# Kernel optimization log

Hardware: AMD Instinct MI355X
Metric: run time of the kernel (lower is better)

## Reference

```python
import jax, jax.numpy as jnp
import numpy as np

BN_EPS = 1e-5

def _batchnorm(z, gamma, beta):
    # training-mode BN over node axis, biased variance (matches torch normalization)
    mean = jnp.mean(z, axis=0)
    var = jnp.mean((z - mean) ** 2, axis=0)
    return (z - mean) * jax.lax.rsqrt(var + BN_EPS) * gamma + beta

def setup_inputs() -> dict:
    key = jax.random.key(0)
    N, E, D, L = 100000, 1000000, 128, 2
    ks = jax.random.split(key, 8)
    x = jax.random.normal(ks[0], (N, D), dtype=jnp.float32)
    edge_index = jax.random.randint(ks[1], (2, E), 0, N, dtype=jnp.int64)
    s = 1.0 / np.sqrt(D)
    W1 = jax.random.uniform(ks[2], (L, D, D), jnp.float32, -s, s)
    b1 = jax.random.uniform(ks[3], (L, D), jnp.float32, -s, s)
    W2 = jax.random.uniform(ks[4], (L, D, D), jnp.float32, -s, s)
    b2 = jax.random.uniform(ks[5], (L, D), jnp.float32, -s, s)
    g1 = jnp.ones((L, D), jnp.float32); bt1 = jnp.zeros((L, D), jnp.float32)
    g_out = jnp.ones((L, D), jnp.float32); bt_out = jnp.zeros((L, D), jnp.float32)
    eps = jnp.zeros((L,), jnp.float32)  # GIN eps, init 0
    return {"x": x, "edge_index": edge_index, "W1": W1, "b1": b1, "g1": g1,
            "bt1": bt1, "W2": W2, "b2": b2, "eps": eps, "g_out": g_out, "bt_out": bt_out}

def reference(x, edge_index, W1, b1, g1, bt1, W2, b2, eps, g_out, bt_out):
    N = x.shape[0]
    L = W1.shape[0]
    src, dst = edge_index[0], edge_index[1]
    h = x
    for l in range(L):
        # message: relu(x_j) gathered along edges; aggregate: scatter-add to dst
        msg = jax.nn.relu(h[src])                                  # [E, D]
        aggr = jax.ops.segment_sum(msg, dst, num_segments=N)       # [N, D]
        z = (1.0 + eps[l]) * h + aggr
        # GINConv MLP: Linear -> BN -> ReLU -> Linear
        z = z @ W1[l].T + b1[l]
        z = jax.nn.relu(_batchnorm(z, g1[l], bt1[l]))
        z = z @ W2[l].T + b2[l]
        # outer per-layer BatchNorm
        z = _batchnorm(z, g_out[l], bt_out[l])
        if l < L - 1:
            z = jax.nn.relu(z)
        # dropout is identity in eval mode
        h = z
    return h
```

## Files before the change

kernel.cpp:

```cpp
#include <hip/hip_runtime.h>

typedef unsigned int u32;
typedef unsigned short u16;
typedef __attribute__((ext_vector_type(8))) short bf16x8;
typedef __attribute__((ext_vector_type(4))) float f32x4;

#define DF 128
#define NBUCK 256
#define BUCK_SHIFT 9
#define BUCK_SIZE 512
#define P2_CHUNK 4096
#define NCOPY 16
#define STATW (NCOPY * DF)

__device__ __forceinline__ float bf2f(u32 h) { return __uint_as_float(h << 16); }
__device__ __forceinline__ u16 f2bf(float f) {
  u32 u = __float_as_uint(f);
  u32 r = (u + 0x7fffu + ((u >> 16) & 1u)) >> 16;
  return (u16)r;
}
__device__ __forceinline__ u32 pack2(float a, float b) {
  return (u32)f2bf(a) | ((u32)f2bf(b) << 16);
}

__global__ void k_cvt3(const float* __restrict__ x, const float* __restrict__ w1,
                       const float* __restrict__ w2, u16* __restrict__ xb,
                       u16* __restrict__ w1b, u16* __restrict__ w2b,
                       int n4x, int n4w) {
  int i = blockIdx.x * blockDim.x + threadIdx.x;
  const float* in; u16* out; int idx;
  if (i < n4x) { in = x; out = xb; idx = i; }
  else if (i < n4x + n4w) { in = w1; out = w1b; idx = i - n4x; }
  else if (i < n4x + 2 * n4w) { in = w2; out = w2b; idx = i - n4x - n4w; }
  else return;
  float4 v = ((const float4*)in)[idx];
  ((uint2*)out)[idx] = make_uint2(pack2(v.x, v.y), pack2(v.z, v.w));
}

__global__ __launch_bounds__(256) void k_p1(const int* __restrict__ dst,
                                            int* __restrict__ bucketCount, int E) {
  __shared__ int h[NBUCK];
  int t = threadIdx.x;
  h[t] = 0;
  __syncthreads();
  for (int e = blockIdx.x * 256 + t; e < E; e += gridDim.x * 256)
    atomicAdd(&h[((u32)dst[e]) >> BUCK_SHIFT], 1);
  __syncthreads();
  if (h[t]) atomicAdd(&bucketCount[t], h[t]);
}

__global__ __launch_bounds__(256) void k_pscan(const int* __restrict__ bucketCount,
                                               int* __restrict__ bucketStart,
                                               int* __restrict__ bucketCursor,
                                               int* __restrict__ rowptr, int N, int E) {
  __shared__ int sh[NBUCK];
  int t = threadIdx.x;
  int c = bucketCount[t];
  sh[t] = c;
  __syncthreads();
  for (int o = 1; o < 256; o <<= 1) {
    int v = (t >= o) ? sh[t - o] : 0;
    __syncthreads();
    sh[t] += v;
    __syncthreads();
  }
  int excl = sh[t] - c;
  bucketStart[t] = excl;
  bucketCursor[t] = excl;
  if (t == 255) { bucketStart[256] = sh[255]; rowptr[N] = E; }
}

__global__ __launch_bounds__(256) void k_p2(const int* __restrict__ src,
                                            const int* __restrict__ dst,
                                            int* __restrict__ bucketCursor,
                                            uint2* __restrict__ part, int E) {
  __shared__ int h[NBUCK], hs[NBUCK], base[NBUCK];
  __shared__ int total;
  __shared__ uint2 buf[P2_CHUNK];
  int t = threadIdx.x;
  int e0 = blockIdx.x * P2_CHUNK;
  h[t] = 0;
  __syncthreads();
  int myb[16], myr[16];
  uint2 mye[16];
  #pragma unroll
  for (int k = 0; k < 16; k++) {
    int e = e0 + k * 256 + t;
    myb[k] = -1;
    if (e < E) {
      int s = src[e], d = dst[e];
      mye[k] = make_uint2((u32)s, (u32)d);
      myb[k] = ((u32)d) >> BUCK_SHIFT;
      myr[k] = atomicAdd(&h[myb[k]], 1);
    }
  }
  __syncthreads();
  int hc = h[t];
  hs[t] = hc;
  __syncthreads();
  for (int o = 1; o < 256; o <<= 1) {
    int v = (t >= o) ? hs[t - o] : 0;
    __syncthreads();
    hs[t] += v;
    __syncthreads();
  }
  if (t == 255) total = hs[255];
  int excl = hs[t] - hc;
  base[t] = hc ? atomicAdd(&bucketCursor[t], hc) : 0;
  __syncthreads();
  hs[t] = excl;
  __syncthreads();
  #pragma unroll
  for (int k = 0; k < 16; k++)
    if (myb[k] >= 0) buf[hs[myb[k]] + myr[k]] = mye[k];
  __syncthreads();
  int tot = total;
  for (int i = t; i < tot; i += 256) {
    uint2 ed = buf[i];
    int b = ed.y >> BUCK_SHIFT;
    part[base[b] + (i - hs[b])] = ed;
  }
}

__global__ __launch_bounds__(256) void k_p3(const uint2* __restrict__ part,
                                            const int* __restrict__ bucketStart,
                                            int* __restrict__ rowptr,
                                            int* __restrict__ adj, int N) {
  __shared__ int deg[BUCK_SIZE], cur[BUCK_SIZE], psum[256];
  int b = blockIdx.x, t = threadIdx.x;
  int nodeBase = b << BUCK_SHIFT;
  int eb = bucketStart[b], ee = bucketStart[b + 1];
  deg[t] = 0; deg[t + 256] = 0;
  __syncthreads();
  for (int e = eb + t; e < ee; e += 256)
    atomicAdd(&deg[(int)part[e].y - nodeBase], 1);
  __syncthreads();
  int a0 = deg[2 * t], a1 = deg[2 * t + 1];
  psum[t] = a0 + a1;
  __syncthreads();
  for (int o = 1; o < 256; o <<= 1) {
    int v = (t >= o) ? psum[t - o] : 0;
    __syncthreads();
    psum[t] += v;
    __syncthreads();
  }
  int basep = psum[t] - (a0 + a1);
  int p0 = eb + basep, p1 = eb + basep + a0;
  cur[2 * t] = p0; cur[2 * t + 1] = p1;
  int n0 = nodeBase + 2 * t, n1 = nodeBase + 2 * t + 1;
  if (n0 < N) rowptr[n0] = p0;
  if (n1 < N) rowptr[n1] = p1;
  __syncthreads();
  for (int e = eb + t; e < ee; e += 256) {
    uint2 ed = part[e];
    int pos = atomicAdd(&cur[(int)ed.y - nodeBase], 1);
    adj[pos] = (int)ed.x;
  }
}

__global__ void k_aggr(const u16* __restrict__ h, const int* __restrict__ rowptr,
                       const int* __restrict__ adj, const float* __restrict__ epsArr,
                       int layer, int doRelu, u16* __restrict__ z, int N) {
  int wid = (blockIdx.x * blockDim.x + threadIdx.x) >> 6;
  if (wid >= N) return;
  int lane = threadIdx.x & 63;
  int g = lane >> 4, f = lane & 15;
  const uint4* h4 = (const uint4*)h;
  float e1 = 1.0f + epsArr[layer];

  f32x4 accLo = {0.f, 0.f, 0.f, 0.f}, accHi = {0.f, 0.f, 0.f, 0.f};

  if (g == 0) {
    uint4 v = h4[(size_t)wid * 16 + f];
    f32x4 lo = {__uint_as_float(v.x << 16), __uint_as_float(v.y << 16),
                __uint_as_float(v.z << 16), __uint_as_float(v.w << 16)};
    f32x4 hi = {__uint_as_float(v.x & 0xffff0000u), __uint_as_float(v.y & 0xffff0000u),
                __uint_as_float(v.z & 0xffff0000u), __uint_as_float(v.w & 0xffff0000u)};
    accLo = e1 * lo;
    accHi = e1 * hi;
  }

  int b = rowptr[wid], e = rowptr[wid + 1];
  for (int p = b; p < e; p += 8) {
    int i0 = p + g, i1 = p + 4 + g;
    uint4 v0 = make_uint4(0, 0, 0, 0), v1 = make_uint4(0, 0, 0, 0);
    if (i0 < e) v0 = h4[(size_t)(u32)adj[i0] * 16 + f];
    if (i1 < e) v1 = h4[(size_t)(u32)adj[i1] * 16 + f];
    u32 w0[4] = {v0.x, v0.y, v0.z, v0.w};
    u32 w1[4] = {v1.x, v1.y, v1.z, v1.w};
    if (doRelu) {
      #pragma unroll
      for (int k = 0; k < 4; k++) {
        u32 a = w0[k];
        if (a & 0x8000u)     a &= 0xffff0000u;
        if (a & 0x80000000u) a &= 0x0000ffffu;
        w0[k] = a;
        u32 bq = w1[k];
        if (bq & 0x8000u)     bq &= 0xffff0000u;
        if (bq & 0x80000000u) bq &= 0x0000ffffu;
        w1[k] = bq;
      }
    }
    f32x4 lo0 = {__uint_as_float(w0[0] << 16), __uint_as_float(w0[1] << 16),
                 __uint_as_float(w0[2] << 16), __uint_as_float(w0[3] << 16)};
    f32x4 hi0 = {__uint_as_float(w0[0] & 0xffff0000u), __uint_as_float(w0[1] & 0xffff0000u),
                 __uint_as_float(w0[2] & 0xffff0000u), __uint_as_float(w0[3] & 0xffff0000u)};
    f32x4 lo1 = {__uint_as_float(w1[0] << 16), __uint_as_float(w1[1] << 16),
                 __uint_as_float(w1[2] << 16), __uint_as_float(w1[3] << 16)};
    f32x4 hi1 = {__uint_as_float(w1[0] & 0xffff0000u), __uint_as_float(w1[1] & 0xffff0000u),
                 __uint_as_float(w1[2] & 0xffff0000u), __uint_as_float(w1[3] & 0xffff0000u)};
    accLo += lo0; accHi += hi0;
    accLo += lo1; accHi += hi1;
  }

  #pragma unroll
  for (int k = 0; k < 4; k++) {
    accLo[k] += __shfl_xor(accLo[k], 16);
    accLo[k] += __shfl_xor(accLo[k], 32);
    accHi[k] += __shfl_xor(accHi[k], 16);
    accHi[k] += __shfl_xor(accHi[k], 32);
  }
  if (g == 0) {
    uint4 o = make_uint4(pack2(accLo[0], accHi[0]), pack2(accLo[1], accHi[1]),
                         pack2(accLo[2], accHi[2]), pack2(accLo[3], accHi[3]));
    ((uint4*)z)[(size_t)wid * 16 + f] = o;
  }
}

__global__ __launch_bounds__(256, 3) void k_gemm(
    const u16* __restrict__ A, const u16* __restrict__ W, const float* __restrict__ bias,
    const float* __restrict__ pS, const float* __restrict__ pQ,
    const float* __restrict__ gamma, const float* __restrict__ beta, int trans,
    float* __restrict__ statS, float* __restrict__ statQ,
    u16* __restrict__ out, int Nrows) {
  __shared__ float sA[DF], sC[DF];
  int tid = threadIdx.x;
  if (trans) {
    if (tid < DF) {
      float S = 0.f, Q = 0.f;
      #pragma unroll
      for (int i = 0; i < NCOPY; i++) { S += pS[i * DF + tid]; Q += pQ[i * DF + tid]; }
      float inv_n = 1.0f / (float)Nrows;
      float mean = S * inv_n;
      float var = fmaxf(Q * inv_n - mean * mean, 0.0f);
      float iv = rsqrtf(var + 1e-5f);
      float av = gamma[tid] * iv;
      sA[tid] = av;
      sC[tid] = beta[tid] - mean * av;
    }
    __syncthreads();
  }

  int lane = tid & 63, w = tid >> 6;
  int rq = w >> 1, cq = w & 1;
  int m = lane & 15, quad = lane >> 4;
  int rowBase = blockIdx.x * 128;
  int lastRow = Nrows - 1;

  f32x4 acc[4][4];
  #pragma unroll
  for (int i = 0; i < 4; i++)
    #pragma unroll
    for (int j = 0; j < 4; j++) acc[i][j] = (f32x4){0.f, 0.f, 0.f, 0.f};

  #pragma unroll
  for (int kt = 0; kt < 4; kt++) {
    int gk = kt * 32 + quad * 8;
    bf16x8 af[4], bfr[4];
    #pragma unroll
    for (int i = 0; i < 4; i++) {
      int row = rowBase + (rq * 4 + i) * 16 + m;
      row = row < Nrows ? row : lastRow;
      af[i] = *(const bf16x8*)(A + (size_t)row * DF + gk);
    }
    #pragma unroll
    for (int j = 0; j < 4; j++)
      bfr[j] = *(const bf16x8*)(W + (size_t)((cq * 4 + j) * 16 + m) * DF + gk);
    if (trans) {
      f32x4 a0 = *(const f32x4*)(sA + gk), a1 = *(const f32x4*)(sA + gk + 4);
      f32x4 c0 = *(const f32x4*)(sC + gk), c1 = *(const f32x4*)(sC + gk + 4);
      #pragma unroll
      for (int i = 0; i < 4; i++) {
        bf16x8 v = af[i];
        #pragma unroll
        for (int k = 0; k < 8; k++) {
          float xk = __uint_as_float(((u32)(u16)v[k]) << 16);
          float ak = (k < 4) ? a0[k] : a1[k - 4];
          float ck = (k < 4) ? c0[k] : c1[k - 4];
          float r = fmaxf(fmaf(ak, xk, ck), 0.0f);
          v[k] = (short)f2bf(r);
        }
        af[i] = v;
      }
    }
    #pragma unroll
    for (int i = 0; i < 4; i++)
      #pragma unroll
      for (int j = 0; j < 4; j++)
        acc[i][j] = __builtin_amdgcn_mfma_f32_16x16x32_bf16(af[i], bfr[j], acc[i][j], 0, 0, 0);
  }

  float colS[4] = {0, 0, 0, 0}, colQ[4] = {0, 0, 0, 0};
  #pragma unroll
  for (int j = 0; j < 4; j++) {
    int col = (cq * 4 + j) * 16 + m;
    float bv = bias[col];
    #pragma unroll
    for (int i = 0; i < 4; i++) {
      int row0 = rowBase + (rq * 4 + i) * 16 + quad * 4;
      #pragma unroll
      for (int r = 0; r < 4; r++) {
        int row = row0 + r;
        if (row < Nrows) {
          float v = acc[i][j][r] + bv;
          out[(size_t)row * DF + col] = f2bf(v);
          colS[j] += v;
          colQ[j] += v * v;
        }
      }
    }
  }
  int copyOff = (blockIdx.x & (NCOPY - 1)) * DF;
  #pragma unroll
  for (int j = 0; j < 4; j++) {
    float s = colS[j], q = colQ[j];
    s += __shfl_xor(s, 16); q += __shfl_xor(q, 16);
    s += __shfl_xor(s, 32); q += __shfl_xor(q, 32);
    if (quad == 0) {
      int col = (cq * 4 + j) * 16 + m;
      atomicAdd(&statS[copyOff + col], s);
      atomicAdd(&statQ[copyOff + col], q);
    }
  }
}

__global__ void k_bnapply_bf16(const u16* __restrict__ u, const float* __restrict__ pS,
                               const float* __restrict__ pQ, const float* __restrict__ gamma,
                               const float* __restrict__ beta, u16* __restrict__ h,
                               int n8, int Nrows) {
  __shared__ float sA[DF], sC[DF];
  int t = threadIdx.x;
  if (t < DF) {
    float S = 0.f, Q = 0.f;
    #pragma unroll
    for (int i = 0; i < NCOPY; i++) { S += pS[i * DF + t]; Q += pQ[i * DF + t]; }
    float inv_n = 1.0f / (float)Nrows;
    float mean = S * inv_n;
    float var = fmaxf(Q * inv_n - mean * mean, 0.0f);
    float iv = rsqrtf(var + 1e-5f);
    float av = gamma[t] * iv;
    sA[t] = av;
    sC[t] = beta[t] - mean * av;
  }
  __syncthreads();
  int i = blockIdx.x * blockDim.x + t;
  if (i >= n8) return;
  int col = (i * 8) & 127;
  f32x4 a0 = *(const f32x4*)(sA + col), a1v = *(const f32x4*)(sA + col + 4);
  f32x4 c0 = *(const f32x4*)(sC + col), c1v = *(const f32x4*)(sC + col + 4);
  uint4 v = ((const uint4*)u)[i];
  float f0 = fmaxf(fmaf(a0[0], bf2f(v.x & 0xffffu), c0[0]), 0.f);
  float f1 = fmaxf(fmaf(a0[1], bf2f(v.x >> 16),     c0[1]), 0.f);
  float f2 = fmaxf(fmaf(a0[2], bf2f(v.y & 0xffffu), c0[2]), 0.f);
  float f3 = fmaxf(fmaf(a0[3], bf2f(v.y >> 16),     c0[3]), 0.f);
  float f4 = fmaxf(fmaf(a1v[0], bf2f(v.z & 0xffffu), c1v[0]), 0.f);
  float f5 = fmaxf(fmaf(a1v[1], bf2f(v.z >> 16),     c1v[1]), 0.f);
  float f6 = fmaxf(fmaf(a1v[2], bf2f(v.w & 0xffffu), c1v[2]), 0.f);
  float f7 = fmaxf(fmaf(a1v[3], bf2f(v.w >> 16),     c1v[3]), 0.f);
  ((uint4*)h)[i] = make_uint4(pack2(f0, f1), pack2(f2, f3), pack2(f4, f5), pack2(f6, f7));
}

__global__ void k_bnapply_f32(const u16* __restrict__ u, const float* __restrict__ pS,
                              const float* __restrict__ pQ, const float* __restrict__ gamma,
                              const float* __restrict__ beta, float* __restrict__ out,
                              int n8, int Nrows) {
  __shared__ float sA[DF], sC[DF];
  int t = threadIdx.x;
  if (t < DF) {
    float S = 0.f, Q = 0.f;
    #pragma unroll
    for (int i = 0; i < NCOPY; i++) { S += pS[i * DF + t]; Q += pQ[i * DF + t]; }
    float inv_n = 1.0f / (float)Nrows;
    float mean = S * inv_n;
    float var = fmaxf(Q * inv_n - mean * mean, 0.0f);
    float iv = rsqrtf(var + 1e-5f);
    float av = gamma[t] * iv;
    sA[t] = av;
    sC[t] = beta[t] - mean * av;
  }
  __syncthreads();
  int i = blockIdx.x * blockDim.x + t;
  if (i >= n8) return;
  int col = (i * 8) & 127;
  f32x4 a0 = *(const f32x4*)(sA + col), a1v = *(const f32x4*)(sA + col + 4);
  f32x4 c0 = *(const f32x4*)(sC + col), c1v = *(const f32x4*)(sC + col + 4);
  uint4 v = ((const uint4*)u)[i];
  float4 o0, o1;
  o0.x = fmaf(a0[0], bf2f(v.x & 0xffffu), c0[0]);
  o0.y = fmaf(a0[1], bf2f(v.x >> 16),     c0[1]);
  o0.z = fmaf(a0[2], bf2f(v.y & 0xffffu), c0[2]);
  o0.w = fmaf(a0[3], bf2f(v.y >> 16),     c0[3]);
  o1.x = fmaf(a1v[0], bf2f(v.z & 0xffffu), c1v[0]);
  o1.y = fmaf(a1v[1], bf2f(v.z >> 16),     c1v[1]);
  o1.z = fmaf(a1v[2], bf2f(v.w & 0xffffu), c1v[2]);
  o1.w = fmaf(a1v[3], bf2f(v.w >> 16),     c1v[3]);
  ((float4*)out)[i * 2] = o0;
  ((float4*)out)[i * 2 + 1] = o1;
}

extern "C" void kernel_launch(void* const* d_in, const int* in_sizes, int n_in,
                              void* d_out, int out_size, void* d_ws, size_t ws_size,
                              hipStream_t stream) {
  const float* x    = (const float*)d_in[0];
  const int*   ei   = (const int*)d_in[1];
  const float* W1   = (const float*)d_in[2];
  const float* b1   = (const float*)d_in[3];
  const float* g1   = (const float*)d_in[4];
  const float* bt1  = (const float*)d_in[5];
  const float* W2   = (const float*)d_in[6];
  const float* b2   = (const float*)d_in[7];
  const float* eps  = (const float*)d_in[8];
  const float* gout = (const float*)d_in[9];
  const float* btout= (const float*)d_in[10];

  int N = in_sizes[0] / DF;
  int E = in_sizes[1] / 2;
  int L = in_sizes[8];

  char* ws = (char*)d_ws;
  size_t off = 0;
  auto alloc = [&](size_t bytes) -> void* {
    void* p = ws + off;
    off += (bytes + 255) & ~(size_t)255;
    return p;
  };
  u16* Xb     = (u16*)alloc((size_t)N * DF * 2);
  u16* bufA   = (u16*)alloc((size_t)N * DF * 2);
  u16* bufB   = (u16*)alloc((size_t)N * DF * 2);
  int* rowptr = (int*)alloc((size_t)(N + 1) * 4);
  int* adj    = (int*)alloc((size_t)E * 4);
  uint2* part = (uint2*)alloc((size_t)E * 8);
  int* bCount = (int*)alloc(NBUCK * 4);
  int* bStart = (int*)alloc((NBUCK + 1) * 4);
  int* bCur   = (int*)alloc(NBUCK * 4);
  u16* W1b    = (u16*)alloc((size_t)L * DF * DF * 2);
  u16* W2b    = (u16*)alloc((size_t)L * DF * DF * 2);
  float* stats= (float*)alloc((size_t)L * 4 * STATW * 4);

  hipMemsetAsync(bCount, 0, NBUCK * 4, stream);
  hipMemsetAsync(stats, 0, (size_t)L * 4 * STATW * 4, stream);

  int n4x = N * DF / 4;
  int n4w = L * DF * DF / 4;
  int n4tot = n4x + 2 * n4w;
  k_cvt3<<<(n4tot + 255) / 256, 256, 0, stream>>>(x, W1, W2, Xb, W1b, W2b, n4x, n4w);

  const int* srcI = ei;
  const int* dstI = ei + E;
  int nbuckets = (N + BUCK_SIZE - 1) >> BUCK_SHIFT;
  k_p1<<<512, 256, 0, stream>>>(dstI, bCount, E);
  k_pscan<<<1, 256, 0, stream>>>(bCount, bStart, bCur, rowptr, N, E);
  k_p2<<<(E + P2_CHUNK - 1) / P2_CHUNK, 256, 0, stream>>>(srcI, dstI, bCur, part, E);
  k_p3<<<nbuckets, 256, 0, stream>>>(part, bStart, rowptr, adj, N);

  int gblocks = (N + 127) / 128;
  int n8 = N * DF / 8;
  for (int l = 0; l < L; l++) {
    float* S1 = stats + (size_t)(l * 4 + 0) * STATW;
    float* Q1 = stats + (size_t)(l * 4 + 1) * STATW;
    float* S2 = stats + (size_t)(l * 4 + 2) * STATW;
    float* Q2 = stats + (size_t)(l * 4 + 3) * STATW;
    const u16* H = (l == 0) ? Xb : bufB;
    k_aggr<<<(N + 3) / 4, 256, 0, stream>>>(H, rowptr, adj, eps, l,
                                            (l == 0) ? 1 : 0, bufA, N);
    k_gemm<<<gblocks, 256, 0, stream>>>(bufA, W1b + l * DF * DF, b1 + l * DF,
                                        nullptr, nullptr, nullptr, nullptr, 0,
                                        S1, Q1, bufB, N);
    k_gemm<<<gblocks, 256, 0, stream>>>(bufB, W2b + l * DF * DF, b2 + l * DF,
                                        S1, Q1, g1 + l * DF, bt1 + l * DF, 1,
                                        S2, Q2, bufA, N);
    if (l < L - 1) {
      k_bnapply_bf16<<<(n8 + 255) / 256, 256, 0, stream>>>(
          bufA, S2, Q2, gout + l * DF, btout + l * DF, bufB, n8, N);
    } else {
      k_bnapply_f32<<<(n8 + 255) / 256, 256, 0, stream>>>(
          bufA, S2, Q2, gout + l * DF, btout + l * DF, (float*)d_out, n8, N);
    }
  }
}
```

Baseline: 449.6 us.

## Fuse neighbor aggregation with first GEMM via shared-memory tile

Result: slower. 563.1 us (+25.2%).

```diff
diff --git a/kernel.cpp b/kernel.cpp
--- a/kernel.cpp
+++ b/kernel.cpp
@@ -6,6 +6,7 @@
 typedef __attribute__((ext_vector_type(4))) float f32x4;
 
 #define DF 128
+#define LDA 136
 #define NBUCK 256
 #define BUCK_SHIFT 9
 #define BUCK_SIZE 512
@@ -158,98 +159,171 @@
   }
 }
 
-__global__ void k_aggr(const u16* __restrict__ h, const int* __restrict__ rowptr,
-                       const int* __restrict__ adj, const float* __restrict__ epsArr,
-                       int layer, int doRelu, u16* __restrict__ z, int N) {
-  int wid = (blockIdx.x * blockDim.x + threadIdx.x) >> 6;
-  if (wid >= N) return;
-  int lane = threadIdx.x & 63;
-  int g = lane >> 4, f = lane & 15;
+__global__ __launch_bounds__(256, 3) void k_aggemm(
+    const u16* __restrict__ h, const int* __restrict__ rowptr,
+    const int* __restrict__ adj, const float* __restrict__ epsArr,
+    int layer, int doRelu,
+    const u16* __restrict__ W, const float* __restrict__ bias,
+    float* __restrict__ statS, float* __restrict__ statQ,
+    u16* __restrict__ out, int N) {
+  __shared__ u16 zt[128 * LDA];
+  int tid = threadIdx.x;
+  int lane = tid & 63, w = tid >> 6;
+  int rowBase = blockIdx.x * 128;
   const uint4* h4 = (const uint4*)h;
   float e1 = 1.0f + epsArr[layer];
 
-  f32x4 accLo = {0.f, 0.f, 0.f, 0.f}, accHi = {0.f, 0.f, 0.f, 0.f};
-
-  if (g == 0) {
-    uint4 v = h4[(size_t)wid * 16 + f];
-    f32x4 lo = {__uint_as_float(v.x << 16), __uint_as_float(v.y << 16),
-                __uint_as_float(v.z << 16), __uint_as_float(v.w << 16)};
-    f32x4 hi = {__uint_as_float(v.x & 0xffff0000u), __uint_as_float(v.y & 0xffff0000u),
-                __uint_as_float(v.z & 0xffff0000u), __uint_as_float(v.w & 0xffff0000u)};
-    accLo = e1 * lo;
-    accHi = e1 * hi;
-  }
-
-  int b = rowptr[wid], e = rowptr[wid + 1];
-  for (int p = b; p < e; p += 8) {
-    int i0 = p + g, i1 = p + 4 + g;
-    uint4 v0 = make_uint4(0, 0, 0, 0), v1 = make_uint4(0, 0, 0, 0);
-    if (i0 < e) v0 = h4[(size_t)(u32)adj[i0] * 16 + f];
-    if (i1 < e) v1 = h4[(size_t)(u32)adj[i1] * 16 + f];
-    u32 w0[4] = {v0.x, v0.y, v0.z, v0.w};
-    u32 w1[4] = {v1.x, v1.y, v1.z, v1.w};
-    if (doRelu) {
+  int nb0w = w * 32;
+  int rpv = 0;
+  {
+    int rpIdx = rowBase + nb0w + lane;
+    if (lane < 33) rpv = rowptr[rpIdx < N ? rpIdx : N];
+  }
+
+  int g = lane >> 4, f = lane & 15;
+  int gl = g & 1;
+  int which = g >> 1;
+
+  for (int j = 0; j < 32; j += 2) {
+    int nb = nb0w + j + which;
+    int node = rowBase + nb;
+    bool valid = (node < N);
+    int b = __shfl(rpv, j + which);
+    int e = __shfl(rpv, j + which + 1);
+    f32x4 accLo = {0.f, 0.f, 0.f, 0.f}, accHi = {0.f, 0.f, 0.f, 0.f};
+
+    if (gl == 0 && valid) {
+      uint4 v = h4[(size_t)node * 16 + f];
+      f32x4 lo = {__uint_as_float(v.x << 16), __uint_as_float(v.y << 16),
+                  __uint_as_float(v.z << 16), __uint_as_float(v.w << 16)};
+      f32x4 hi = {__uint_as_float(v.x & 0xffff0000u), __uint_as_float(v.y & 0xffff0000u),
+                  __uint_as_float(v.z & 0xffff0000u), __uint_as_float(v.w & 0xffff0000u)};
+      accLo = e1 * lo;
+      accHi = e1 * hi;
+    }
+
+    for (int p = b; p < e; p += 4) {
+      int i0 = p + gl, i1 = p + 2 + gl;
+      uint4 v0 = make_uint4(0, 0, 0, 0), v1 = make_uint4(0, 0, 0, 0);
+      if (i0 < e) v0 = h4[(size_t)(u32)adj[i0] * 16 + f];
+      if (i1 < e) v1 = h4[(size_t)(u32)adj[i1] * 16 + f];
+      u32 w0[4] = {v0.x, v0.y, v0.z, v0.w};
+      u32 w1[4] = {v1.x, v1.y, v1.z, v1.w};
+      if (doRelu) {
+        #pragma unroll
+        for (int k = 0; k < 4; k++) {
+          u32 a = w0[k];
+          if (a & 0x8000u)     a &= 0xffff0000u;
+          if (a & 0x80000000u) a &= 0x0000ffffu;
+          w0[k] = a;
+          u32 bq = w1[k];
+          if (bq & 0x8000u)     bq &= 0xffff0000u;
+          if (bq & 0x80000000u) bq &= 0x0000ffffu;
+          w1[k] = bq;
+        }
+      }
       #pragma unroll
       for (int k = 0; k < 4; k++) {
-        u32 a = w0[k];
-        if (a & 0x8000u)     a &= 0xffff0000u;
-        if (a & 0x80000000u) a &= 0x0000ffffu;
-        w0[k] = a;
-        u32 bq = w1[k];
-        if (bq & 0x8000u)     bq &= 0xffff0000u;
-        if (bq & 0x80000000u) bq &= 0x0000ffffu;
-        w1[k] = bq;
+        accLo[k] += __uint_as_float(w0[k] << 16);
+        accHi[k] += __uint_as_float(w0[k] & 0xffff0000u);
+        accLo[k] += __uint_as_float(w1[k] << 16);
+        accHi[k] += __uint_as_float(w1[k] & 0xffff0000u);
       }
     }
-    f32x4 lo0 = {__uint_as_float(w0[0] << 16), __uint_as_float(w0[1] << 16),
-                 __uint_as_float(w0[2] << 16), __uint_as_float(w0[3] << 16)};
-    f32x4 hi0 = {__uint_as_float(w0[0] & 0xffff0000u), __uint_as_float(w0[1] & 0xffff0000u),
-                 __uint_as_float(w0[2] & 0xffff0000u), __uint_as_float(w0[3] & 0xffff0000u)};
-    f32x4 lo1 = {__uint_as_float(w1[0] << 16), __uint_as_float(w1[1] << 16),
-                 __uint_as_float(w1[2] << 16), __uint_as_float(w1[3] << 16)};
-    f32x4 hi1 = {__uint_as_float(w1[0] & 0xffff0000u), __uint_as_float(w1[1] & 0xffff0000u),
-                 __uint_as_float(w1[2] & 0xffff0000u), __uint_as_float(w1[3] & 0xffff0000u)};
-    accLo += lo0; accHi += hi0;
-    accLo += lo1; accHi += hi1;
-  }
-
-  #pragma unroll
-  for (int k = 0; k < 4; k++) {
-    accLo[k] += __shfl_xor(accLo[k], 16);
-    accLo[k] += __shfl_xor(accLo[k], 32);
-    accHi[k] += __shfl_xor(accHi[k], 16);
-    accHi[k] += __shfl_xor(accHi[k], 32);
-  }
-  if (g == 0) {
-    uint4 o = make_uint4(pack2(accLo[0], accHi[0]), pack2(accLo[1], accHi[1]),
-                         pack2(accLo[2], accHi[2]), pack2(accLo[3], accHi[3]));
-    ((uint4*)z)[(size_t)wid * 16 + f] = o;
+
+    #pragma unroll
+    for (int k = 0; k < 4; k++) {
+      accLo[k] += __shfl_xor(accLo[k], 16);
+      accHi[k] += __shfl_xor(accHi[k], 16);
+    }
+    if (gl == 0) {
+      uint4 o = make_uint4(pack2(accLo[0], accHi[0]), pack2(accLo[1], accHi[1]),
+                           pack2(accLo[2], accHi[2]), pack2(accLo[3], accHi[3]));
+      *(uint4*)(&zt[(size_t)nb * LDA + f * 8]) = o;
+    }
+  }
+  __syncthreads();
+
+  int rq = w >> 1, cq = w & 1;
+  int m = lane & 15, quad = lane >> 4;
+  f32x4 acc[4][4];
+  #pragma unroll
+  for (int i = 0; i < 4; i++)
+    #pragma unroll
+    for (int j = 0; j < 4; j++) acc[i][j] = (f32x4){0.f, 0.f, 0.f, 0.f};
+
+  #pragma unroll
+  for (int kt = 0; kt < 4; kt++) {
+    int gk = kt * 32 + quad * 8;
+    bf16x8 af[4], bfr[4];
+    #pragma unroll
+    for (int i = 0; i < 4; i++)
+      af[i] = *(const bf16x8*)(&zt[(size_t)((rq * 4 + i) * 16 + m) * LDA + gk]);
+    #pragma unroll
+    for (int j = 0; j < 4; j++)
+      bfr[j] = *(const bf16x8*)(W + (size_t)((cq * 4 + j) * 16 + m) * DF + gk);
+    #pragma unroll
+    for (int i = 0; i < 4; i++)
+      #pragma unroll
+      for (int j = 0; j < 4; j++)
+        acc[i][j] = __builtin_amdgcn_mfma_f32_16x16x32_bf16(af[i], bfr[j], acc[i][j], 0, 0, 0);
+  }
+
+  float colS[4] = {0, 0, 0, 0}, colQ[4] = {0, 0, 0, 0};
+  #pragma unroll
+  for (int j = 0; j < 4; j++) {
+    int col = (cq * 4 + j) * 16 + m;
+    float bv = bias[col];
+    #pragma unroll
+    for (int i = 0; i < 4; i++) {
+      int row0 = rowBase + (rq * 4 + i) * 16 + quad * 4;
+      #pragma unroll
+      for (int r = 0; r < 4; r++) {
+        int row = row0 + r;
+        if (row < N) {
+          float v = acc[i][j][r] + bv;
+          out[(size_t)row * DF + col] = f2bf(v);
+          colS[j] += v;
+          colQ[j] += v * v;
+        }
+      }
+    }
+  }
+  int copyOff = (blockIdx.x & (NCOPY - 1)) * DF;
+  #pragma unroll
+  for (int j = 0; j < 4; j++) {
+    float s = colS[j], q = colQ[j];
+    s += __shfl_xor(s, 16); q += __shfl_xor(q, 16);
+    s += __shfl_xor(s, 32); q += __shfl_xor(q, 32);
+    if (quad == 0) {
+      int col = (cq * 4 + j) * 16 + m;
+      atomicAdd(&statS[copyOff + col], s);
+      atomicAdd(&statQ[copyOff + col], q);
+    }
   }
 }
 
 __global__ __launch_bounds__(256, 3) void k_gemm(
     const u16* __restrict__ A, const u16* __restrict__ W, const float* __restrict__ bias,
     const float* __restrict__ pS, const float* __restrict__ pQ,
-    const float* __restrict__ gamma, const float* __restrict__ beta, int trans,
+    const float* __restrict__ gamma, const float* __restrict__ beta,
     float* __restrict__ statS, float* __restrict__ statQ,
     u16* __restrict__ out, int Nrows) {
   __shared__ float sA[DF], sC[DF];
   int tid = threadIdx.x;
-  if (trans) {
-    if (tid < DF) {
-      float S = 0.f, Q = 0.f;
-      #pragma unroll
-      for (int i = 0; i < NCOPY; i++) { S += pS[i * DF + tid]; Q += pQ[i * DF + tid]; }
-      float inv_n = 1.0f / (float)Nrows;
-      float mean = S * inv_n;
-      float var = fmaxf(Q * inv_n - mean * mean, 0.0f);
-      float iv = rsqrtf(var + 1e-5f);
-      float av = gamma[tid] * iv;
-      sA[tid] = av;
-      sC[tid] = beta[tid] - mean * av;
-    }
-    __syncthreads();
-  }
+  if (tid < DF) {
+    float S = 0.f, Q = 0.f;
+    #pragma unroll
+    for (int i = 0; i < NCOPY; i++) { S += pS[i * DF + tid]; Q += pQ[i * DF + tid]; }
+    float inv_n = 1.0f / (float)Nrows;
+    float mean = S * inv_n;
+    float var = fmaxf(Q * inv_n - mean * mean, 0.0f);
+    float iv = rsqrtf(var + 1e-5f);
+    float av = gamma[tid] * iv;
+    sA[tid] = av;
+    sC[tid] = beta[tid] - mean * av;
+  }
+  __syncthreads();
 
   int lane = tid & 63, w = tid >> 6;
   int rq = w >> 1, cq = w & 1;
@@ -276,22 +350,20 @@
     #pragma unroll
     for (int j = 0; j < 4; j++)
       bfr[j] = *(const bf16x8*)(W + (size_t)((cq * 4 + j) * 16 + m) * DF + gk);
-    if (trans) {
-      f32x4 a0 = *(const f32x4*)(sA + gk), a1 = *(const f32x4*)(sA + gk + 4);
-      f32x4 c0 = *(const f32x4*)(sC + gk), c1 = *(const f32x4*)(sC + gk + 4);
+    f32x4 a0 = *(const f32x4*)(sA + gk), a1 = *(const f32x4*)(sA + gk + 4);
+    f32x4 c0 = *(const f32x4*)(sC + gk), c1 = *(const f32x4*)(sC + gk + 4);
+    #pragma unroll
+    for (int i = 0; i < 4; i++) {
+      bf16x8 v = af[i];
       #pragma unroll
-      for (int i = 0; i < 4; i++) {
-        bf16x8 v = af[i];
-        #pragma unroll
-        for (int k = 0; k < 8; k++) {
-          float xk = __uint_as_float(((u32)(u16)v[k]) << 16);
-          float ak = (k < 4) ? a0[k] : a1[k - 4];
-          float ck = (k < 4) ? c0[k] : c1[k - 4];
-          float r = fmaxf(fmaf(ak, xk, ck), 0.0f);
-          v[k] = (short)f2bf(r);
-        }
-        af[i] = v;
+      for (int k = 0; k < 8; k++) {
+        float xk = __uint_as_float(((u32)(u16)v[k]) << 16);
+        float ak = (k < 4) ? a0[k] : a1[k - 4];
+        float ck = (k < 4) ? c0[k] : c1[k - 4];
+        float r = fmaxf(fmaf(ak, xk, ck), 0.0f);
+        v[k] = (short)f2bf(r);
       }
+      af[i] = v;
     }
     #pragma unroll
     for (int i = 0; i < 4; i++)
@@ -470,21 +542,18 @@
     float* Q1 = stats + (size_t)(l * 4 + 1) * STATW;
     float* S2 = stats + (size_t)(l * 4 + 2) * STATW;
     float* Q2 = stats + (size_t)(l * 4 + 3) * STATW;
-    const u16* H = (l == 0) ? Xb : bufB;
-    k_aggr<<<(N + 3) / 4, 256, 0, stream>>>(H, rowptr, adj, eps, l,
-                                            (l == 0) ? 1 : 0, bufA, N);
-    k_gemm<<<gblocks, 256, 0, stream>>>(bufA, W1b + l * DF * DF, b1 + l * DF,
-                                        nullptr, nullptr, nullptr, nullptr, 0,
-                                        S1, Q1, bufB, N);
-    k_gemm<<<gblocks, 256, 0, stream>>>(bufB, W2b + l * DF * DF, b2 + l * DF,
-                                        S1, Q1, g1 + l * DF, bt1 + l * DF, 1,
-                                        S2, Q2, bufA, N);
+    k_aggemm<<<gblocks, 256, 0, stream>>>(Xb, rowptr, adj, eps, l, (l == 0) ? 1 : 0,
+                                          W1b + l * DF * DF, b1 + l * DF,
+                                          S1, Q1, bufA, N);
+    k_gemm<<<gblocks, 256, 0, stream>>>(bufA, W2b + l * DF * DF, b2 + l * DF,
+                                        S1, Q1, g1 + l * DF, bt1 + l * DF,
+                                        S2, Q2, bufB, N);
     if (l < L - 1) {
       k_bnapply_bf16<<<(n8 + 255) / 256, 256, 0, stream>>>(
-          bufA, S2, Q2, gout + l * DF, btout + l * DF, bufB, n8, N);
+          bufB, S2, Q2, gout + l * DF, btout + l * DF, Xb, n8, N);
     } else {
       k_bnapply_f32<<<(n8 + 255) / 256, 256, 0, stream>>>(
-          bufA, S2, Q2, gout + l * DF, btout + l * DF, (float*)d_out, n8, N);
-    }
-  }
-}
+          bufB, S2, Q2, gout + l * DF, btout + l * DF, (float*)d_out, n8, N);
+    }
+  }
+}
```
